# Kernel tuning notes

Hardware: AMD Instinct MI355X
Metric: run time of the kernel (lower is better)

Reference implementation:

```python
import jax, jax.numpy as jnp
import numpy as np

DIM = 1024
NUM_HEADS = 16
SCALE = DIM ** (-0.5)  # NOTE: source scales by full dim, not head_dim


def setup_inputs() -> dict:
    key = jax.random.key(0)
    ks = jax.random.split(key, 10)
    B, N, C = 2, 2048, DIM
    s = 0.02
    return {
        "x": jax.random.normal(ks[0], (B, N, C), dtype=jnp.float32),
        "queries": jax.random.normal(ks[1], (B, N, C), dtype=jnp.float32),
        "wq": jax.random.normal(ks[2], (C, C), dtype=jnp.float32) * s,
        "bq": jnp.zeros((C,), dtype=jnp.float32),
        "wk": jax.random.normal(ks[3], (C, C), dtype=jnp.float32) * s,
        "bk": jnp.zeros((C,), dtype=jnp.float32),
        "wv": jax.random.normal(ks[4], (C, C), dtype=jnp.float32) * s,
        "bv": jnp.zeros((C,), dtype=jnp.float32),
        "wo": jax.random.normal(ks[5], (C, C), dtype=jnp.float32) * s,
        "bo": jnp.zeros((C,), dtype=jnp.float32),
    }


def reference(x, queries, wq, bq, wk, bk, wv, bv, wo, bo):
    B, N, C = queries.shape
    H = NUM_HEADS
    D = C // H
    # torch Linear: y = x @ W.T + b  (W is [out, in])
    q = (queries @ wq.T + bq).reshape(B, N, H, D).transpose(0, 2, 1, 3)  # [B,H,N,D]
    k = (x @ wk.T + bk).reshape(B, N, H, D).transpose(0, 2, 1, 3)
    v = (x @ wv.T + bv).reshape(B, N, H, D).transpose(0, 2, 1, 3)
    attn = jnp.einsum("bhqd,bhkd->bhqk", q, k) * SCALE  # full-dim scale per source
    attn = jax.nn.softmax(attn, axis=-1)
    out = jnp.einsum("bhqk,bhkd->bhqd", attn, v)  # [B,H,N,D]
    out = out.transpose(0, 2, 1, 3).reshape(B, N, C)
    return out @ wo.T + bo
```

## Files before the change

### kernel.cpp

```cpp
#include <hip/hip_runtime.h>
#include <hip/hip_bf16.h>

typedef __attribute__((ext_vector_type(8))) short bf16x8;
typedef __attribute__((ext_vector_type(4))) float f32x4;
typedef unsigned short u16;
typedef unsigned int u32;

#define MFMA16(a,b,c) __builtin_amdgcn_mfma_f32_16x16x32_bf16((a),(b),(c),0,0,0)

#if defined(__has_builtin) && __has_builtin(__builtin_amdgcn_exp2f)
#define EXP2(x) __builtin_amdgcn_exp2f(x)
#else
#define EXP2(x) exp2f(x)
#endif

#define QSCALE 0.045084220027780106f

__device__ __forceinline__ u16 f2bf(float f) {
  union { float f; unsigned int u; } v; v.f = f;
  unsigned int r = v.u + 0x7FFFu + ((v.u >> 16) & 1u);
  return (u16)(r >> 16);
}

__device__ __forceinline__ u32 pkbf(float a, float b) {
  union { __hip_bfloat162 h; u32 u; } cv;
  cv.h = __float22bfloat162_rn(make_float2(a, b));
  return cv.u;
}

__device__ __forceinline__ void gld16(const void* g, void* l) {
  __builtin_amdgcn_global_load_lds(
      (__attribute__((address_space(1))) void*)(g),
      (__attribute__((address_space(3))) void*)(l), 16, 0, 0);
}

__global__ __launch_bounds__(256) void cast_all(
    const float* __restrict__ x, const float* __restrict__ qu,
    const float* __restrict__ wq, const float* __restrict__ wk,
    const float* __restrict__ wv, const float* __restrict__ wo,
    u16* __restrict__ xb, u16* __restrict__ qub,
    u16* __restrict__ wqb, u16* __restrict__ wkb,
    u16* __restrict__ wvb, u16* __restrict__ wob)
{
  int i = blockIdx.x * 256 + threadIdx.x;
  const float4* src; u16* dst; int off;
  if (i < 1048576)      { src = (const float4*)qu; dst = qub; off = i; }
  else if (i < 2097152) { src = (const float4*)x;  dst = xb;  off = i - 1048576; }
  else if (i < 2359296) { src = (const float4*)wq; dst = wqb; off = i - 2097152; }
  else if (i < 2621440) { src = (const float4*)wk; dst = wkb; off = i - 2359296; }
  else if (i < 2883584) { src = (const float4*)wv; dst = wvb; off = i - 2621440; }
  else                  { src = (const float4*)wo; dst = wob; off = i - 2883584; }
  float4 v = src[off];
  ushort4 r; r.x = f2bf(v.x); r.y = f2bf(v.y); r.z = f2bf(v.z); r.w = f2bf(v.w);
  ((ushort4*)dst)[off] = r;
}

__global__ __launch_bounds__(256) void gemm_qkv(
    const u16* __restrict__ qub, const u16* __restrict__ xb,
    const u16* __restrict__ wqb, const u16* __restrict__ wkb, const u16* __restrict__ wvb,
    const float* __restrict__ bq, const float* __restrict__ bk, const float* __restrict__ bv,
    u16* __restrict__ qhd, u16* __restrict__ khd, u16* __restrict__ vtd)
{
  __shared__ u16 As[128 * 64];
  __shared__ u16 Bs[128 * 64];
  int tid = threadIdx.x, w = tid >> 6, lane = tid & 63;
  int c = lane & 15, quad = lane >> 4;
  int bm = blockIdx.x, bn = blockIdx.y, z = blockIdx.z;
  int wm = w >> 1, wn = w & 1;
  const u16* A = (z == 0) ? qub : xb;
  const u16* W = (z == 0) ? wqb : (z == 1) ? wkb : wvb;
  f32x4 acc[4][4] = {};
  for (int k0 = 0; k0 < 1024; k0 += 64) {
#pragma unroll
    for (int i = 0; i < 4; i++) {
      int seg = i * 256 + w * 64 + lane;
      int row = seg >> 3, pseg = seg & 7;
      int lseg = pseg ^ (row & 7);
      gld16(A + (size_t)(bm * 128 + row) * 1024 + k0 + lseg * 8,
            &As[(i * 256 + w * 64) * 8]);
      gld16(W + (size_t)(bn * 128 + row) * 1024 + k0 + lseg * 8,
            &Bs[(i * 256 + w * 64) * 8]);
    }
    __syncthreads();
#pragma unroll
    for (int ks = 0; ks < 2; ks++) {
      bf16x8 af[4], bfr[4];
#pragma unroll
      for (int mt = 0; mt < 4; mt++) {
        int row = wm * 64 + mt * 16 + c;
        int cseg = (ks * 4 + quad) ^ (row & 7);
        af[mt] = *(const bf16x8*)&As[(row * 8 + cseg) * 8];
      }
#pragma unroll
      for (int nt = 0; nt < 4; nt++) {
        int row = wn * 64 + nt * 16 + c;
        int cseg = (ks * 4 + quad) ^ (row & 7);
        bfr[nt] = *(const bf16x8*)&Bs[(row * 8 + cseg) * 8];
      }
      if (z < 2) {
#pragma unroll
        for (int ct = 0; ct < 4; ct++)
#pragma unroll
          for (int tt = 0; tt < 4; tt++)
            acc[ct][tt] = MFMA16(bfr[ct], af[tt], acc[ct][tt]);
      } else {
#pragma unroll
        for (int mt = 0; mt < 4; mt++)
#pragma unroll
          for (int nt = 0; nt < 4; nt++)
            acc[mt][nt] = MFMA16(af[mt], bfr[nt], acc[mt][nt]);
      }
    }
    __syncthreads();
  }
  if (z < 2) {
    const float* bias = (z == 0) ? bq : bk;
    u16* dst = (z == 0) ? qhd : khd;
    float sc = (z == 0) ? QSCALE : 1.0f;
    float4 bbs[4];
#pragma unroll
    for (int ct = 0; ct < 4; ct++) {
      float4 b4 = *(const float4*)&bias[bn * 128 + wn * 64 + ct * 16 + quad * 4];
      bbs[ct].x = b4.x * sc; bbs[ct].y = b4.y * sc;
      bbs[ct].z = b4.z * sc; bbs[ct].w = b4.w * sc;
    }
#pragma unroll
    for (int ct = 0; ct < 4; ct++) {
      int ch = bn * 128 + wn * 64 + ct * 16 + quad * 4;
      int h = ch >> 6, d0 = ch & 63;
#pragma unroll
      for (int tt = 0; tt < 4; tt++) {
        int tok = bm * 128 + wm * 64 + tt * 16 + c;
        int b = tok >> 11, n = tok & 2047;
        float v0 = fmaf(acc[ct][tt][0], sc, bbs[ct].x);
        float v1 = fmaf(acc[ct][tt][1], sc, bbs[ct].y);
        float v2 = fmaf(acc[ct][tt][2], sc, bbs[ct].z);
        float v3 = fmaf(acc[ct][tt][3], sc, bbs[ct].w);
        uint2 pk; pk.x = pkbf(v0, v1); pk.y = pkbf(v2, v3);
        *(uint2*)&dst[((size_t)(b * 16 + h) * 2048 + n) * 64 + d0] = pk;
      }
    }
  } else {
    float bval[4];
#pragma unroll
    for (int nt = 0; nt < 4; nt++)
      bval[nt] = bv[bn * 128 + wn * 64 + nt * 16 + c];
#pragma unroll
    for (int mt = 0; mt < 4; mt++) {
      int tokl = (mt & 2) * 16 + quad * 8 + (mt & 1) * 4;
      int tok = bm * 128 + wm * 64 + tokl;
      int b = tok >> 11, np = tok & 2047;
#pragma unroll
      for (int nt = 0; nt < 4; nt++) {
        int ch = bn * 128 + wn * 64 + nt * 16 + c;
        int h = ch >> 6, d = ch & 63;
        float v0 = acc[mt][nt][0] + bval[nt];
        float v1 = acc[mt][nt][1] + bval[nt];
        float v2 = acc[mt][nt][2] + bval[nt];
        float v3 = acc[mt][nt][3] + bval[nt];
        uint2 pk; pk.x = pkbf(v0, v1); pk.y = pkbf(v2, v3);
        *(uint2*)&vtd[((size_t)(b * 16 + h) * 64 + d) * 2048 + np] = pk;
      }
    }
  }
}

__global__ __launch_bounds__(128, 2) void attn(
    const u16* __restrict__ qh, const u16* __restrict__ kh,
    const u16* __restrict__ vt, u16* __restrict__ ot)
{
  __shared__ u16 KL[2][2][32 * 64];
  __shared__ u16 VL[2][2][64 * 32];
  __shared__ float CL[64];
  int tid = threadIdx.x, w = tid >> 6, lane = tid & 63;
  int c = lane & 15, quad = lane >> 4;
  int bh = blockIdx.x, qt = blockIdx.y;

  const u16* qp = qh + ((size_t)bh * 2048 + qt * 64) * 64;
  bf16x8 Qf[4][2];
#pragma unroll
  for (int q2 = 0; q2 < 4; q2++)
#pragma unroll
    for (int ks = 0; ks < 2; ks++)
      Qf[q2][ks] = *(const bf16x8*)(qp + (size_t)(q2 * 16 + c) * 64 + ks * 32 + quad * 8);

  int kro = lane >> 3;
  int ksw = ((lane & 7) ^ (kro & 7)) * 8;
  const u16* kg = kh + (size_t)bh * 131072 + (size_t)w * 65536 + kro * 64 + ksw;
  int vro = lane >> 2;
  int vsw = ((lane & 3) ^ (vro & 3)) * 8;
  const u16* vg = vt + (size_t)bh * 131072 + (size_t)vro * 2048 + w * 1024 + vsw;

  int off0 = c * 64 + ((quad) ^ (c & 7)) * 8;
  int off1 = c * 64 + ((4 + quad) ^ (c & 7)) * 8;
  int offV = c * 32 + ((quad ^ (c & 3)) & 3) * 8;

#define STAGE(B)                                                                \
  {                                                                             \
    gld16(kg,          &KL[w][B][0]);                                           \
    gld16(kg + 512,    &KL[w][B][512]);                                         \
    gld16(kg + 1024,   &KL[w][B][1024]);                                        \
    gld16(kg + 1536,   &KL[w][B][1536]);                                        \
    gld16(vg,          &VL[w][B][0]);                                           \
    gld16(vg + 32768,  &VL[w][B][512]);                                         \
    gld16(vg + 65536,  &VL[w][B][1024]);                                        \
    gld16(vg + 98304,  &VL[w][B][1536]);                                        \
    kg += 2048; vg += 32;                                                       \
  }

  f32x4 O[4][4] = {};
  f32x4 Lacc[4] = {};
  bf16x8 vone;
#pragma unroll
  for (int j = 0; j < 8; j++) vone[j] = (short)0x3F80;

#define ITER(PH, PREF)                                                          \
  {                                                                             \
    asm volatile("s_waitcnt lgkmcnt(0)" ::: "memory");                          \
    __builtin_amdgcn_sched_barrier(0);                                          \
    if (PREF) STAGE(PH ^ 1)                                                     \
    if (PREF) { asm volatile("s_waitcnt vmcnt(8)" ::: "memory"); }              \
    else      { asm volatile("s_waitcnt vmcnt(0)" ::: "memory"); }              \
    __builtin_amdgcn_sched_barrier(0);                                          \
    const u16* Ks = KL[w][PH];                                                  \
    const u16* Vs = VL[w][PH];                                                  \
    bf16x8 Kf[2][2];                                                            \
    Kf[0][0] = *(const bf16x8*)&Ks[off0];                                       \
    Kf[0][1] = *(const bf16x8*)&Ks[off1];                                       \
    Kf[1][0] = *(const bf16x8*)&Ks[off0 + 1024];                                \
    Kf[1][1] = *(const bf16x8*)&Ks[off1 + 1024];                                \
    f32x4 S[4][2] = {};                                                         \
    _Pragma("unroll") for (int q2 = 0; q2 < 4; q2++)                            \
      _Pragma("unroll") for (int nt = 0; nt < 2; nt++) {                        \
        S[q2][nt] = MFMA16(Kf[nt][0], Qf[q2][0], S[q2][nt]);                    \
        S[q2][nt] = MFMA16(Kf[nt][1], Qf[q2][1], S[q2][nt]);                    \
      }                                                                         \
    bf16x8 pa[4];                                                               \
    _Pragma("unroll") for (int q2 = 0; q2 < 4; q2++) {                          \
      float e0 = EXP2(S[q2][0][0]), e1 = EXP2(S[q2][0][1]);                     \
      float e2 = EXP2(S[q2][0][2]), e3 = EXP2(S[q2][0][3]);                     \
      float e4 = EXP2(S[q2][1][0]), e5 = EXP2(S[q2][1][1]);                     \
      float e6 = EXP2(S[q2][1][2]), e7 = EXP2(S[q2][1][3]);                     \
      union { uint4 u; bf16x8 v; } cv;                                          \
      cv.u.x = pkbf(e0, e1); cv.u.y = pkbf(e2, e3);                             \
      cv.u.z = pkbf(e4, e5); cv.u.w = pkbf(e6, e7);                             \
      pa[q2] = cv.v;                                                            \
    }                                                                           \
    bf16x8 Vf[4];                                                               \
    Vf[0] = *(const bf16x8*)&Vs[offV];                                          \
    Vf[1] = *(const bf16x8*)&Vs[offV + 512];                                    \
    Vf[2] = *(const bf16x8*)&Vs[offV + 1024];                                   \
    Vf[3] = *(const bf16x8*)&Vs[offV + 1536];                                   \
    Lacc[0] = MFMA16(pa[0], vone, Lacc[0]);                                     \
    Lacc[1] = MFMA16(pa[1], vone, Lacc[1]);                                     \
    Lacc[2] = MFMA16(pa[2], vone, Lacc[2]);                                     \
    Lacc[3] = MFMA16(pa[3], vone, Lacc[3]);                                     \
    _Pragma("unroll") for (int q2 = 0; q2 < 4; q2++)                            \
      _Pragma("unroll") for (int dt = 0; dt < 4; dt++)                          \
        O[q2][dt] = MFMA16(pa[q2], Vf[dt], O[q2][dt]);                          \
  }

  STAGE(0)
  for (int t2 = 0; t2 < 15; t2++) {
    ITER(0, 1)
    ITER(1, 1)
  }
  ITER(0, 1)
  ITER(1, 0)
#undef ITER
#undef STAGE

  __syncthreads();
  float* CmbO = (float*)&KL[0][0][0];
  if (w == 1) {
#pragma unroll
    for (int q2 = 0; q2 < 4; q2++) {
      if (c == 0)
        *(f32x4*)&CL[q2 * 16 + quad * 4] = Lacc[q2];
#pragma unroll
      for (int dt = 0; dt < 4; dt++)
#pragma unroll
        for (int j = 0; j < 4; j++)
          CmbO[(q2 * 16 + quad * 4 + j) * 64 + dt * 16 + c] = O[q2][dt][j];
    }
  }
  __syncthreads();
  if (w == 0) {
    int b_ = bh >> 4, h = bh & 15;
#pragma unroll
    for (int q2 = 0; q2 < 4; q2++) {
#pragma unroll
      for (int j = 0; j < 4; j++) {
        int qrow = q2 * 16 + quad * 4 + j;
        float ltot = Lacc[q2][j] + CL[qrow];
        float linv = 1.0f / ltot;
        int n = qt * 64 + qrow;
        u16* op = ot + (((size_t)b_ * 2048 + n) * 16 + h) * 64;
#pragma unroll
        for (int dt = 0; dt < 4; dt++) {
          float o = O[q2][dt][j] + CmbO[qrow * 64 + dt * 16 + c];
          op[dt * 16 + c] = f2bf(o * linv);
        }
      }
    }
  }
}

__global__ __launch_bounds__(256) void gemm_out(
    const u16* __restrict__ Aot, const u16* __restrict__ wob,
    const float* __restrict__ bo, float* __restrict__ out)
{
  __shared__ u16 As[64 * 64];
  __shared__ u16 Bs[128 * 64];
  int tid = threadIdx.x, w = tid >> 6, lane = tid & 63;
  int bm = blockIdx.x, bn = blockIdx.y;
  int wm = w >> 1, wn = w & 1;
  f32x4 acc[2][4] = {};
  for (int k0 = 0; k0 < 1024; k0 += 64) {
#pragma unroll
    for (int i = 0; i < 2; i++) {
      int seg = i * 256 + tid;
      int row = seg >> 3, pseg = seg & 7;
      int lseg = pseg ^ (row & 7);
      gld16(Aot + (size_t)(bm * 64 + row) * 1024 + k0 + lseg * 8,
            &As[(i * 256 + tid - (tid & 7)) * 8 + (tid & 7) * 8]);
    }
#pragma unroll
    for (int i = 0; i < 4; i++) {
      int seg = i * 256 + tid;
      int row = seg >> 3, pseg = seg & 7;
      int lseg = pseg ^ (row & 7);
      gld16(wob + (size_t)(bn * 128 + row) * 1024 + k0 + lseg * 8,
            &Bs[(i * 256 + tid - (tid & 7)) * 8 + (tid & 7) * 8]);
    }
    __syncthreads();
#pragma unroll
    for (int ks = 0; ks < 2; ks++) {
      bf16x8 af[2], bfr[4];
#pragma unroll
      for (int mt = 0; mt < 2; mt++) {
        int row = wm * 32 + mt * 16 + (lane & 15);
        int cseg = (ks * 4 + (lane >> 4)) ^ (row & 7);
        af[mt] = *(const bf16x8*)&As[(row * 8 + cseg) * 8];
      }
#pragma unroll
      for (int nt = 0; nt < 4; nt++) {
        int row = wn * 64 + nt * 16 + (lane & 15);
        int cseg = (ks * 4 + (lane >> 4)) ^ (row & 7);
        bfr[nt] = *(const bf16x8*)&Bs[(row * 8 + cseg) * 8];
      }
#pragma unroll
      for (int mt = 0; mt < 2; mt++)
#pragma unroll
        for (int nt = 0; nt < 4; nt++)
          acc[mt][nt] = MFMA16(af[mt], bfr[nt], acc[mt][nt]);
    }
    __syncthreads();
  }
#pragma unroll
  for (int nt = 0; nt < 4; nt++) {
    int o = bn * 128 + wn * 64 + nt * 16 + (lane & 15);
    float bval = bo[o];
#pragma unroll
    for (int mt = 0; mt < 2; mt++)
#pragma unroll
      for (int j = 0; j < 4; j++) {
        int m = bm * 64 + wm * 32 + mt * 16 + (lane >> 4) * 4 + j;
        out[(size_t)m * 1024 + o] = acc[mt][nt][j] + bval;
      }
  }
}

extern "C" void kernel_launch(void* const* d_in, const int* in_sizes, int n_in,
                              void* d_out, int out_size, void* d_ws, size_t ws_size,
                              hipStream_t stream)
{
  const float* x  = (const float*)d_in[0];
  const float* qu = (const float*)d_in[1];
  const float* wq = (const float*)d_in[2];
  const float* bq = (const float*)d_in[3];
  const float* wk = (const float*)d_in[4];
  const float* bk = (const float*)d_in[5];
  const float* wv = (const float*)d_in[6];
  const float* bv = (const float*)d_in[7];
  const float* wo = (const float*)d_in[8];
  const float* bo = (const float*)d_in[9];
  float* out = (float*)d_out;
  char* ws = (char*)d_ws;
  u16* xb  = (u16*)(ws + (size_t)0);
  u16* qub = (u16*)(ws + ((size_t)8  << 20));
  u16* wqb = (u16*)(ws + ((size_t)16 << 20));
  u16* wkb = (u16*)(ws + ((size_t)18 << 20));
  u16* wvb = (u16*)(ws + ((size_t)20 << 20));
  u16* wob = (u16*)(ws + ((size_t)22 << 20));
  u16* qhd = (u16*)(ws + ((size_t)24 << 20));
  u16* khd = (u16*)(ws + ((size_t)32 << 20));
  u16* vtd = (u16*)(ws + ((size_t)40 << 20));
  u16* otd = (u16*)(ws + ((size_t)48 << 20));

  cast_all<<<12288, 256, 0, stream>>>(x, qu, wq, wk, wv, wo,
                                      xb, qub, wqb, wkb, wvb, wob);
  gemm_qkv<<<dim3(32, 8, 3), 256, 0, stream>>>(qub, xb, wqb, wkb, wvb,
                                               bq, bk, bv, qhd, khd, vtd);
  attn<<<dim3(32, 32), 128, 0, stream>>>(qhd, khd, vtd, otd);
  gemm_out<<<dim3(64, 8), 256, 0, stream>>>(otd, wob, bo, out);
}
```

Before: 201.5 us.

## Software-pipeline QK^T of next tile with softmax-PV of current tile

Restructures the attention inner loop into BUILD and CONSUME stages with double-buffered score and V-fragment registers. The QK^T MFMAs and V loads for the next KV tile are issued before the exp/PV work of the current tile, so MFMA latency overlaps with transcendental math. It also prefetches two stages up front. The extra live register sets (two S and Vf sets) raise VGPR pressure, which risks spills or lower occupancy. The buffer-reuse ordering around LDS stages is delicate.

```diff
diff --git a/kernel.cpp b/kernel.cpp
--- a/kernel.cpp
+++ b/kernel.cpp
@@ -208,66 +208,83 @@
     kg += 2048; vg += 32;                                                       \
   }
 
+#define LGKM0 { asm volatile("s_waitcnt lgkmcnt(0)" ::: "memory");              \
+                __builtin_amdgcn_sched_barrier(0); }
+#define WAITV8 { asm volatile("s_waitcnt vmcnt(8)" ::: "memory");               \
+                 __builtin_amdgcn_sched_barrier(0); }
+#define WAITV0 { asm volatile("s_waitcnt vmcnt(0)" ::: "memory");               \
+                 __builtin_amdgcn_sched_barrier(0); }
+
+  const f32x4 zz = {};
   f32x4 O[4][4] = {};
   f32x4 Lacc[4] = {};
+  f32x4 SA[4][2], SB[4][2];
+  bf16x8 VfA[4], VfB[4];
   bf16x8 vone;
 #pragma unroll
   for (int j = 0; j < 8; j++) vone[j] = (short)0x3F80;
 
-#define ITER(PH, PREF)                                                          \
+#define BUILD(Sx, Vfx, PH)                                                      \
   {                                                                             \
-    asm volatile("s_waitcnt lgkmcnt(0)" ::: "memory");                          \
-    __builtin_amdgcn_sched_barrier(0);                                          \
-    if (PREF) STAGE(PH ^ 1)                                                     \
-    if (PREF) { asm volatile("s_waitcnt vmcnt(8)" ::: "memory"); }              \
-    else      { asm volatile("s_waitcnt vmcnt(0)" ::: "memory"); }              \
-    __builtin_amdgcn_sched_barrier(0);                                          \
     const u16* Ks = KL[w][PH];                                                  \
     const u16* Vs = VL[w][PH];                                                  \
-    bf16x8 Kf[2][2];                                                            \
-    Kf[0][0] = *(const bf16x8*)&Ks[off0];                                       \
-    Kf[0][1] = *(const bf16x8*)&Ks[off1];                                       \
-    Kf[1][0] = *(const bf16x8*)&Ks[off0 + 1024];                                \
-    Kf[1][1] = *(const bf16x8*)&Ks[off1 + 1024];                                \
-    f32x4 S[4][2] = {};                                                         \
-    _Pragma("unroll") for (int q2 = 0; q2 < 4; q2++)                            \
-      _Pragma("unroll") for (int nt = 0; nt < 2; nt++) {                        \
-        S[q2][nt] = MFMA16(Kf[nt][0], Qf[q2][0], S[q2][nt]);                    \
-        S[q2][nt] = MFMA16(Kf[nt][1], Qf[q2][1], S[q2][nt]);                    \
-      }                                                                         \
-    bf16x8 pa[4];                                                               \
+    bf16x8 Kf00 = *(const bf16x8*)&Ks[off0];                                    \
+    bf16x8 Kf01 = *(const bf16x8*)&Ks[off1];                                    \
+    bf16x8 Kf10 = *(const bf16x8*)&Ks[off0 + 1024];                             \
+    bf16x8 Kf11 = *(const bf16x8*)&Ks[off1 + 1024];                             \
+    Vfx[0] = *(const bf16x8*)&Vs[offV];                                         \
+    Vfx[1] = *(const bf16x8*)&Vs[offV + 512];                                   \
+    Vfx[2] = *(const bf16x8*)&Vs[offV + 1024];                                  \
+    Vfx[3] = *(const bf16x8*)&Vs[offV + 1536];                                  \
     _Pragma("unroll") for (int q2 = 0; q2 < 4; q2++) {                          \
-      float e0 = EXP2(S[q2][0][0]), e1 = EXP2(S[q2][0][1]);                     \
-      float e2 = EXP2(S[q2][0][2]), e3 = EXP2(S[q2][0][3]);                     \
-      float e4 = EXP2(S[q2][1][0]), e5 = EXP2(S[q2][1][1]);                     \
-      float e6 = EXP2(S[q2][1][2]), e7 = EXP2(S[q2][1][3]);                     \
+      Sx[q2][0] = MFMA16(Kf01, Qf[q2][1], MFMA16(Kf00, Qf[q2][0], zz));         \
+      Sx[q2][1] = MFMA16(Kf11, Qf[q2][1], MFMA16(Kf10, Qf[q2][0], zz));         \
+    }                                                                           \
+  }
+
+#define CONSUME(Sx, Vfx)                                                        \
+  {                                                                             \
+    _Pragma("unroll") for (int q2 = 0; q2 < 4; q2++) {                          \
+      float e0 = EXP2(Sx[q2][0][0]), e1 = EXP2(Sx[q2][0][1]);                   \
+      float e2 = EXP2(Sx[q2][0][2]), e3 = EXP2(Sx[q2][0][3]);                   \
+      float e4 = EXP2(Sx[q2][1][0]), e5 = EXP2(Sx[q2][1][1]);                   \
+      float e6 = EXP2(Sx[q2][1][2]), e7 = EXP2(Sx[q2][1][3]);                   \
       union { uint4 u; bf16x8 v; } cv;                                          \
       cv.u.x = pkbf(e0, e1); cv.u.y = pkbf(e2, e3);                             \
       cv.u.z = pkbf(e4, e5); cv.u.w = pkbf(e6, e7);                             \
-      pa[q2] = cv.v;                                                            \
+      bf16x8 pa = cv.v;                                                         \
+      Lacc[q2] = MFMA16(pa, vone, Lacc[q2]);                                    \
+      _Pragma("unroll") for (int dt = 0; dt < 4; dt++)                          \
+        O[q2][dt] = MFMA16(pa, Vfx[dt], O[q2][dt]);                             \
     }                                                                           \
-    bf16x8 Vf[4];                                                               \
-    Vf[0] = *(const bf16x8*)&Vs[offV];                                          \
-    Vf[1] = *(const bf16x8*)&Vs[offV + 512];                                    \
-    Vf[2] = *(const bf16x8*)&Vs[offV + 1024];                                   \
-    Vf[3] = *(const bf16x8*)&Vs[offV + 1536];                                   \
-    Lacc[0] = MFMA16(pa[0], vone, Lacc[0]);                                     \
-    Lacc[1] = MFMA16(pa[1], vone, Lacc[1]);                                     \
-    Lacc[2] = MFMA16(pa[2], vone, Lacc[2]);                                     \
-    Lacc[3] = MFMA16(pa[3], vone, Lacc[3]);                                     \
-    _Pragma("unroll") for (int q2 = 0; q2 < 4; q2++)                            \
-      _Pragma("unroll") for (int dt = 0; dt < 4; dt++)                          \
-        O[q2][dt] = MFMA16(pa[q2], Vf[dt], O[q2][dt]);                          \
   }
 
   STAGE(0)
-  for (int t2 = 0; t2 < 15; t2++) {
-    ITER(0, 1)
-    ITER(1, 1)
-  }
-  ITER(0, 1)
-  ITER(1, 0)
-#undef ITER
+  STAGE(1)
+  WAITV8
+  BUILD(SA, VfA, 0)
+
+  for (int hp = 0; hp < 15; hp++) {
+    LGKM0
+    STAGE(0)
+    WAITV8
+    BUILD(SB, VfB, 1)
+    CONSUME(SA, VfA)
+    LGKM0
+    STAGE(1)
+    WAITV8
+    BUILD(SA, VfA, 0)
+    CONSUME(SB, VfB)
+  }
+  WAITV0
+  BUILD(SB, VfB, 1)
+  CONSUME(SA, VfA)
+  CONSUME(SB, VfB)
+#undef CONSUME
+#undef BUILD
+#undef WAITV0
+#undef WAITV8
+#undef LGKM0
 #undef STAGE
 
   __syncthreads();
```

Measured after the change: 203.5 us. Within noise of the previous version (+1.0%).

## Double-buffer LDS tiles in QKV and output projection GEMMs

Applied to the files above, without the earlier changes.

Both projection GEMMs now keep two LDS buffers and issue the global-to-LDS async loads for the next K tile before computing on the current one. Partial vmcnt waits and sched barriers let the current tile's loads complete while the next tile's loads stay in flight, hiding global memory latency behind MFMA work. The cost is double the LDS footprint (64KB for gemm_qkv), which may reduce occupancy, and the loop relies on hand-counted vmcnt values.

```diff
diff --git a/kernel.cpp b/kernel.cpp
--- a/kernel.cpp
+++ b/kernel.cpp
@@ -33,6 +33,9 @@
       (__attribute__((address_space(1))) void*)(g),
       (__attribute__((address_space(3))) void*)(l), 16, 0, 0);
 }
+
+#define SB __builtin_amdgcn_sched_barrier(0);
+#define BARR  SB __builtin_amdgcn_s_barrier(); SB
 
 __global__ __launch_bounds__(256) void cast_all(
     const float* __restrict__ x, const float* __restrict__ qu,
@@ -61,8 +64,8 @@
     const float* __restrict__ bq, const float* __restrict__ bk, const float* __restrict__ bv,
     u16* __restrict__ qhd, u16* __restrict__ khd, u16* __restrict__ vtd)
 {
-  __shared__ u16 As[128 * 64];
-  __shared__ u16 Bs[128 * 64];
+  __shared__ u16 As[2][128 * 64];
+  __shared__ u16 Bs[2][128 * 64];
   int tid = threadIdx.x, w = tid >> 6, lane = tid & 63;
   int c = lane & 15, quad = lane >> 4;
   int bm = blockIdx.x, bn = blockIdx.y, z = blockIdx.z;
@@ -70,49 +73,64 @@
   const u16* A = (z == 0) ? qub : xb;
   const u16* W = (z == 0) ? wqb : (z == 1) ? wkb : wvb;
   f32x4 acc[4][4] = {};
-  for (int k0 = 0; k0 < 1024; k0 += 64) {
-#pragma unroll
-    for (int i = 0; i < 4; i++) {
-      int seg = i * 256 + w * 64 + lane;
-      int row = seg >> 3, pseg = seg & 7;
-      int lseg = pseg ^ (row & 7);
-      gld16(A + (size_t)(bm * 128 + row) * 1024 + k0 + lseg * 8,
-            &As[(i * 256 + w * 64) * 8]);
-      gld16(W + (size_t)(bn * 128 + row) * 1024 + k0 + lseg * 8,
-            &Bs[(i * 256 + w * 64) * 8]);
-    }
-    __syncthreads();
-#pragma unroll
-    for (int ks = 0; ks < 2; ks++) {
-      bf16x8 af[4], bfr[4];
-#pragma unroll
-      for (int mt = 0; mt < 4; mt++) {
-        int row = wm * 64 + mt * 16 + c;
-        int cseg = (ks * 4 + quad) ^ (row & 7);
-        af[mt] = *(const bf16x8*)&As[(row * 8 + cseg) * 8];
-      }
-#pragma unroll
-      for (int nt = 0; nt < 4; nt++) {
-        int row = wn * 64 + nt * 16 + c;
-        int cseg = (ks * 4 + quad) ^ (row & 7);
-        bfr[nt] = *(const bf16x8*)&Bs[(row * 8 + cseg) * 8];
-      }
-      if (z < 2) {
-#pragma unroll
-        for (int ct = 0; ct < 4; ct++)
-#pragma unroll
-          for (int tt = 0; tt < 4; tt++)
-            acc[ct][tt] = MFMA16(bfr[ct], af[tt], acc[ct][tt]);
-      } else {
-#pragma unroll
-        for (int mt = 0; mt < 4; mt++)
-#pragma unroll
-          for (int nt = 0; nt < 4; nt++)
-            acc[mt][nt] = MFMA16(af[mt], bfr[nt], acc[mt][nt]);
-      }
-    }
-    __syncthreads();
-  }
+
+#define QSTAGE(B, K0)                                                           \
+  {                                                                             \
+    _Pragma("unroll") for (int i = 0; i < 4; i++) {                             \
+      int seg = i * 256 + w * 64 + lane;                                        \
+      int row = seg >> 3, pseg = seg & 7;                                       \
+      int lseg = pseg ^ (row & 7);                                              \
+      gld16(A + (size_t)(bm * 128 + row) * 1024 + (K0) + lseg * 8,              \
+            &As[B][(i * 256 + w * 64) * 8]);                                    \
+      gld16(W + (size_t)(bn * 128 + row) * 1024 + (K0) + lseg * 8,              \
+            &Bs[B][(i * 256 + w * 64) * 8]);                                    \
+    }                                                                           \
+  }
+
+#define QCOMP(PH)                                                               \
+  {                                                                             \
+    _Pragma("unroll") for (int ks = 0; ks < 2; ks++) {                          \
+      bf16x8 af[4], bfr[4];                                                     \
+      _Pragma("unroll") for (int mt = 0; mt < 4; mt++) {                        \
+        int row = wm * 64 + mt * 16 + c;                                        \
+        int cseg = (ks * 4 + quad) ^ (row & 7);                                 \
+        af[mt] = *(const bf16x8*)&As[PH][(row * 8 + cseg) * 8];                 \
+      }                                                                         \
+      _Pragma("unroll") for (int nt = 0; nt < 4; nt++) {                        \
+        int row = wn * 64 + nt * 16 + c;                                        \
+        int cseg = (ks * 4 + quad) ^ (row & 7);                                 \
+        bfr[nt] = *(const bf16x8*)&Bs[PH][(row * 8 + cseg) * 8];                \
+      }                                                                         \
+      if (z < 2) {                                                              \
+        _Pragma("unroll") for (int ct = 0; ct < 4; ct++)                        \
+          _Pragma("unroll") for (int tt = 0; tt < 4; tt++)                      \
+            acc[ct][tt] = MFMA16(bfr[ct], af[tt], acc[ct][tt]);                 \
+      } else {                                                                  \
+        _Pragma("unroll") for (int mt = 0; mt < 4; mt++)                        \
+          _Pragma("unroll") for (int nt = 0; nt < 4; nt++)                      \
+            acc[mt][nt] = MFMA16(af[mt], bfr[nt], acc[mt][nt]);                 \
+      }                                                                         \
+    }                                                                           \
+  }
+
+#define WV8 { SB asm volatile("s_waitcnt vmcnt(8)" ::: "memory"); SB }
+#define WV0 { SB asm volatile("s_waitcnt vmcnt(0)" ::: "memory"); SB }
+
+  QSTAGE(0, 0)
+  int k0 = 64;
+  for (int kk = 0; kk < 7; kk++) {
+    BARR QSTAGE(1, k0) WV8 BARR QCOMP(0)
+    k0 += 64;
+    BARR QSTAGE(0, k0) WV8 BARR QCOMP(1)
+    k0 += 64;
+  }
+  BARR QSTAGE(1, 960) WV8 BARR QCOMP(0)
+  BARR WV0 BARR QCOMP(1)
+#undef WV0
+#undef WV8
+#undef QCOMP
+#undef QSTAGE
+
   if (z < 2) {
     const float* bias = (z == 0) ? bq : bk;
     u16* dst = (z == 0) ? qhd : khd;
@@ -310,53 +328,69 @@
     const u16* __restrict__ Aot, const u16* __restrict__ wob,
     const float* __restrict__ bo, float* __restrict__ out)
 {
-  __shared__ u16 As[64 * 64];
-  __shared__ u16 Bs[128 * 64];
+  __shared__ u16 As[2][64 * 64];
+  __shared__ u16 Bs[2][128 * 64];
   int tid = threadIdx.x, w = tid >> 6, lane = tid & 63;
   int bm = blockIdx.x, bn = blockIdx.y;
   int wm = w >> 1, wn = w & 1;
   f32x4 acc[2][4] = {};
-  for (int k0 = 0; k0 < 1024; k0 += 64) {
-#pragma unroll
-    for (int i = 0; i < 2; i++) {
-      int seg = i * 256 + tid;
-      int row = seg >> 3, pseg = seg & 7;
-      int lseg = pseg ^ (row & 7);
-      gld16(Aot + (size_t)(bm * 64 + row) * 1024 + k0 + lseg * 8,
-            &As[(i * 256 + tid - (tid & 7)) * 8 + (tid & 7) * 8]);
-    }
-#pragma unroll
-    for (int i = 0; i < 4; i++) {
-      int seg = i * 256 + tid;
-      int row = seg >> 3, pseg = seg & 7;
-      int lseg = pseg ^ (row & 7);
-      gld16(wob + (size_t)(bn * 128 + row) * 1024 + k0 + lseg * 8,
-            &Bs[(i * 256 + tid - (tid & 7)) * 8 + (tid & 7) * 8]);
-    }
-    __syncthreads();
-#pragma unroll
-    for (int ks = 0; ks < 2; ks++) {
-      bf16x8 af[2], bfr[4];
-#pragma unroll
-      for (int mt = 0; mt < 2; mt++) {
-        int row = wm * 32 + mt * 16 + (lane & 15);
-        int cseg = (ks * 4 + (lane >> 4)) ^ (row & 7);
-        af[mt] = *(const bf16x8*)&As[(row * 8 + cseg) * 8];
-      }
-#pragma unroll
-      for (int nt = 0; nt < 4; nt++) {
-        int row = wn * 64 + nt * 16 + (lane & 15);
-        int cseg = (ks * 4 + (lane >> 4)) ^ (row & 7);
-        bfr[nt] = *(const bf16x8*)&Bs[(row * 8 + cseg) * 8];
-      }
-#pragma unroll
-      for (int mt = 0; mt < 2; mt++)
-#pragma unroll
-        for (int nt = 0; nt < 4; nt++)
-          acc[mt][nt] = MFMA16(af[mt], bfr[nt], acc[mt][nt]);
-    }
-    __syncthreads();
-  }
+
+#define OSTAGE(B, K0)                                                           \
+  {                                                                             \
+    _Pragma("unroll") for (int i = 0; i < 2; i++) {                             \
+      int seg = i * 256 + tid;                                                  \
+      int row = seg >> 3, pseg = seg & 7;                                       \
+      int lseg = pseg ^ (row & 7);                                              \
+      gld16(Aot + (size_t)(bm * 64 + row) * 1024 + (K0) + lseg * 8,             \
+            &As[B][(i * 256 + tid) * 8]);                                       \
+    }                                                                           \
+    _Pragma("unroll") for (int i = 0; i < 4; i++) {                             \
+      int seg = i * 256 + tid;                                                  \
+      int row = seg >> 3, pseg = seg & 7;                                       \
+      int lseg = pseg ^ (row & 7);                                              \
+      gld16(wob + (size_t)(bn * 128 + row) * 1024 + (K0) + lseg * 8,            \
+            &Bs[B][(i * 256 + tid) * 8]);                                       \
+    }                                                                           \
+  }
+
+#define OCOMP(PH)                                                               \
+  {                                                                             \
+    _Pragma("unroll") for (int ks = 0; ks < 2; ks++) {                          \
+      bf16x8 af[2], bfr[4];                                                     \
+      _Pragma("unroll") for (int mt = 0; mt < 2; mt++) {                        \
+        int row = wm * 32 + mt * 16 + (lane & 15);                              \
+        int cseg = (ks * 4 + (lane >> 4)) ^ (row & 7);                          \
+        af[mt] = *(const bf16x8*)&As[PH][(row * 8 + cseg) * 8];                 \
+      }                                                                         \
+      _Pragma("unroll") for (int nt = 0; nt < 4; nt++) {                        \
+        int row = wn * 64 + nt * 16 + (lane & 15);                              \
+        int cseg = (ks * 4 + (lane >> 4)) ^ (row & 7);                          \
+        bfr[nt] = *(const bf16x8*)&Bs[PH][(row * 8 + cseg) * 8];                \
+      }                                                                         \
+      _Pragma("unroll") for (int mt = 0; mt < 2; mt++)                          \
+        _Pragma("unroll") for (int nt = 0; nt < 4; nt++)                        \
+          acc[mt][nt] = MFMA16(af[mt], bfr[nt], acc[mt][nt]);                   \
+    }                                                                           \
+  }
+
+#define WV6 { SB asm volatile("s_waitcnt vmcnt(6)" ::: "memory"); SB }
+#define WV0 { SB asm volatile("s_waitcnt vmcnt(0)" ::: "memory"); SB }
+
+  OSTAGE(0, 0)
+  int k0 = 64;
+  for (int kk = 0; kk < 7; kk++) {
+    BARR OSTAGE(1, k0) WV6 BARR OCOMP(0)
+    k0 += 64;
+    BARR OSTAGE(0, k0) WV6 BARR OCOMP(1)
+    k0 += 64;
+  }
+  BARR OSTAGE(1, 960) WV6 BARR OCOMP(0)
+  BARR WV0 BARR OCOMP(1)
+#undef WV0
+#undef WV6
+#undef OCOMP
+#undef OSTAGE
+
 #pragma unroll
   for (int nt = 0; nt < 4; nt++) {
     int o = bn * 128 + wn * 64 + nt * 16 + (lane & 15);
```

After: 202.5 us. About the same (+0.5%).
